# Performance work log

Measured on AMD Instinct MI355X. Metric: run time of the kernel, lower is better.

## Reference

```python
import jax, jax.numpy as jnp
import numpy as np
from jax import lax

B_SZ, SEQ, D_MODEL = 8, 2048, 1024
N_LAYER = 2
D_INNER = 2 * D_MODEL          # expand=2
D_STATE = 16
D_CONV = 4
DT_RANK = D_MODEL // 16        # ceil(1024/16)=64
EPS = 1e-5


def setup_inputs() -> dict:
    key = jax.random.key(0)
    ks = jax.random.split(key, 8)
    f = lambda k, shp, sc: jax.random.normal(k, shp, jnp.float32) * sc
    A_log = jnp.tile(jnp.log(jnp.arange(1, D_STATE + 1, dtype=jnp.float32)),
                     (N_LAYER, D_INNER, 1))  # S4D-real init, [L, d_inner, d_state]
    return {
        "x": f(ks[0], (B_SZ, SEQ, D_MODEL), 1.0),
        "in_proj_w": f(ks[1], (N_LAYER, 2 * D_INNER, D_MODEL), 0.02),
        "conv_w": f(ks[2], (N_LAYER, D_INNER, D_CONV), 0.2),
        "conv_b": jnp.zeros((N_LAYER, D_INNER), jnp.float32),
        "x_proj_w": f(ks[3], (N_LAYER, DT_RANK + 2 * D_STATE, D_INNER), 0.02),
        "dt_proj_w": f(ks[4], (N_LAYER, D_INNER, DT_RANK), 0.1),
        "dt_proj_b": f(ks[5], (N_LAYER, D_INNER), 0.5) - 4.0,  # softplus -> small dt
        "A_log": A_log,
        "D_param": jnp.ones((N_LAYER, D_INNER), jnp.float32),
        "out_proj_w": f(ks[6], (N_LAYER, D_MODEL, D_INNER), 0.02),
        "norm_w": jnp.ones((N_LAYER, D_MODEL), jnp.float32),
        "norm_b": jnp.zeros((N_LAYER, D_MODEL), jnp.float32),
    }


def _layer_norm(x, w, b):
    mu = jnp.mean(x, axis=-1, keepdims=True)
    var = jnp.mean(jnp.square(x - mu), axis=-1, keepdims=True)
    return (x - mu) * lax.rsqrt(var + EPS) * w + b


def _causal_dw_conv(x, w, b):
    # x: [B, Lq, d_inner], w: [d_inner, d_conv] depthwise causal conv
    xp = jnp.pad(x, ((0, 0), (D_CONV - 1, 0), (0, 0)))
    L = x.shape[1]
    y = b
    for k in range(D_CONV):
        y = y + xp[:, k:k + L, :] * w[:, k]
    return y


def _selective_scan(u, dt, Bm, Cm, A, Dp):
    # u, dt: [B, Lq, d_inner]; Bm, Cm: [B, Lq, d_state]; A: [d_inner, d_state]
    def step(h, inp):
        ut, dtt, Bt, Ct = inp                         # [B,di],[B,di],[B,ds],[B,ds]
        dA = jnp.exp(dtt[..., None] * A)              # [B, di, ds]
        h = dA * h + (dtt * ut)[..., None] * Bt[:, None, :]
        y = jnp.einsum('bds,bs->bd', h, Ct)
        return h, y

    h0 = jnp.zeros((u.shape[0], D_INNER, D_STATE), u.dtype)
    xs = (u.transpose(1, 0, 2), dt.transpose(1, 0, 2),
          Bm.transpose(1, 0, 2), Cm.transpose(1, 0, 2))
    _, ys = lax.scan(step, h0, xs)                    # ys: [Lq, B, di]
    return ys.transpose(1, 0, 2) + u * Dp


def _mamba(x, in_w, cw, cb, xpw, dtw, dtb, A_log, Dp, ow):
    xz = jnp.einsum('bld,ed->ble', x, in_w)           # [B, L, 2*d_inner]
    xi, z = jnp.split(xz, 2, axis=-1)
    xc = jax.nn.silu(_causal_dw_conv(xi, cw, cb))     # [B, L, d_inner]
    xdbl = jnp.einsum('bld,ed->ble', xc, xpw)         # [B, L, dt_rank+2*d_state]
    dt_low = xdbl[..., :DT_RANK]
    Bm = xdbl[..., DT_RANK:DT_RANK + D_STATE]
    Cm = xdbl[..., DT_RANK + D_STATE:]
    dt = jax.nn.softplus(jnp.einsum('blr,dr->bld', dt_low, dtw) + dtb)
    A = -jnp.exp(A_log)                               # [d_inner, d_state]
    y = _selective_scan(xc, dt, Bm, Cm, A, Dp)
    y = y * jax.nn.silu(z)
    return jnp.einsum('ble,de->bld', y, ow)           # [B, L, d_model]


def reference(x, in_proj_w, conv_w, conv_b, x_proj_w, dt_proj_w, dt_proj_b,
              A_log, D_param, out_proj_w, norm_w, norm_b):
    residual = None
    for l in range(N_LAYER):
        residual = x if residual is None else x + residual
        h = _layer_norm(residual, norm_w[l], norm_b[l])
        x = _mamba(h, in_proj_w[l], conv_w[l], conv_b[l], x_proj_w[l],
                   dt_proj_w[l], dt_proj_b[l], A_log[l], D_param[l], out_proj_w[l])
    # NOTE: source forward returns x without applying norm_f
    return x
```

## Files before the change

kernel.cpp:

```cpp
#include <hip/hip_runtime.h>
#include <cstddef>
#include <cstdint>

#define SEQB   8
#define SEQL   2048
#define DMODEL 1024
#define DINNER 2048
#define DSTATE 16
#define NC     32
#define TC     64
#define TT     8

typedef __attribute__((ext_vector_type(4))) float f32x4;
typedef __attribute__((ext_vector_type(8))) short bf16x8;
typedef unsigned int u32;
typedef const __attribute__((address_space(1))) u32* gas_ptr;
typedef __attribute__((address_space(3))) u32* las_ptr;

__device__ __forceinline__ void gld16(const void* g, void* l){
  __builtin_amdgcn_global_load_lds((gas_ptr)g, (las_ptr)l, 16, 0, 0);
}

__device__ __forceinline__ float siluf(float x){ return x / (1.f + __expf(-x)); }
__device__ __forceinline__ float softplusf(float x){ return (x > 20.f) ? x : log1pf(__expf(x)); }

__device__ __forceinline__ unsigned short f2bf_rne(float f){
  unsigned int u = __float_as_uint(f);
  u += 0x7FFFu + ((u>>16)&1u);
  return (unsigned short)(u>>16);
}
__device__ __forceinline__ void split_bf(float f, unsigned short& h, unsigned short& l){
  unsigned short hs = f2bf_rne(f);
  float hf = __uint_as_float(((unsigned int)hs)<<16);
  h = hs;
  l = f2bf_rne(f - hf);
}

#define CV8P(PH, PSRC) { \
  const float4* _p4 = (const float4*)(PSRC); \
  float4 _a = _p4[0], _b = _p4[1]; \
  bf16x8 _H, _L; unsigned short _h,_l; \
  split_bf(_a.x,_h,_l); _H[0]=(short)_h; _L[0]=(short)_l; \
  split_bf(_a.y,_h,_l); _H[1]=(short)_h; _L[1]=(short)_l; \
  split_bf(_a.z,_h,_l); _H[2]=(short)_h; _L[2]=(short)_l; \
  split_bf(_a.w,_h,_l); _H[3]=(short)_h; _L[3]=(short)_l; \
  split_bf(_b.x,_h,_l); _H[4]=(short)_h; _L[4]=(short)_l; \
  split_bf(_b.y,_h,_l); _H[5]=(short)_h; _L[5]=(short)_l; \
  split_bf(_b.z,_h,_l); _H[6]=(short)_h; _L[6]=(short)_l; \
  split_bf(_b.w,_h,_l); _H[7]=(short)_h; _L[7]=(short)_l; \
  *(bf16x8*)(PH) = _H; *(bf16x8*)((unsigned short*)(PH) + 64) = _L; }

__global__ __launch_bounds__(256)
void wsplit2(const float* __restrict__ src, unsigned short* __restrict__ dst,
             int K, int k4shift)
{
  int idx = blockIdx.x*256 + threadIdx.x;
  int r  = idx >> k4shift;
  int c4 = idx & ((1<<k4shift)-1);
  float4 v = ((const float4*)src)[idx];
  unsigned short h,l; short4 h4, l4;
  split_bf(v.x,h,l); h4.x=(short)h; l4.x=(short)l;
  split_bf(v.y,h,l); h4.y=(short)h; l4.y=(short)l;
  split_bf(v.z,h,l); h4.z=(short)h; l4.z=(short)l;
  split_bf(v.w,h,l); h4.w=(short)h; l4.w=(short)l;
  size_t ro = (size_t)r*2*K;
  *(short4*)&dst[ro + (c4<<2)]     = h4;
  *(short4*)&dst[ro + K + (c4<<2)] = l4;
}

__global__ __launch_bounds__(256)
void wsplit_og(const float* __restrict__ src, unsigned short* __restrict__ dst)
{
  int idx = blockIdx.x*256 + threadIdx.x;
  int r  = idx >> 9;
  int c4 = idx & 511;
  int layer = r >> 10, rr = r & 1023;
  float4 v = ((const float4*)src)[idx];
  unsigned short h,l; short4 h4, l4;
  split_bf(v.x,h,l); h4.x=(short)h; l4.x=(short)l;
  split_bf(v.y,h,l); h4.y=(short)h; l4.y=(short)l;
  split_bf(v.z,h,l); h4.z=(short)h; l4.z=(short)l;
  split_bf(v.w,h,l); h4.w=(short)h; l4.w=(short)l;
  int col = c4 << 2;
  int g = col >> 8, j = col & 255;
  size_t base = (size_t)layer*1024*4096 + (size_t)rr*4096 + g*512 + j;
  *(short4*)&dst[base]       = h4;
  *(short4*)&dst[base + 256] = l4;
}

__global__ __launch_bounds__(256)
void ln_split2(const float* __restrict__ a, const float* __restrict__ res,
               const float* __restrict__ w, const float* __restrict__ bias,
               unsigned short* __restrict__ Hs)
{
  int row = blockIdx.x;
  size_t off = (size_t)row * DMODEL;
  float4 v = ((const float4*)(a + off))[threadIdx.x];
  if (res){
    float4 u = ((const float4*)(res + off))[threadIdx.x];
    v.x += u.x; v.y += u.y; v.z += u.z; v.w += u.w;
  }
  float s  = v.x + v.y + v.z + v.w;
  float s2 = fmaf(v.x,v.x, fmaf(v.y,v.y, fmaf(v.z,v.z, v.w*v.w)));
  #pragma unroll
  for (int o=32;o>0;o>>=1){ s += __shfl_down(s,o,64); s2 += __shfl_down(s2,o,64); }
  __shared__ float red[8];
  int lane = threadIdx.x & 63, wid = threadIdx.x >> 6;
  if (lane==0){ red[wid]=s; red[4+wid]=s2; }
  __syncthreads();
  s  = red[0]+red[1]+red[2]+red[3];
  s2 = red[4]+red[5]+red[6]+red[7];
  float mu  = s * (1.f/DMODEL);
  float var = s2 * (1.f/DMODEL) - mu*mu;
  float rstd = rsqrtf(var + 1e-5f);
  float4 wv = ((const float4*)w)[threadIdx.x];
  float4 bv = ((const float4*)bias)[threadIdx.x];
  float4 o4;
  o4.x = (v.x-mu)*rstd*wv.x + bv.x;
  o4.y = (v.y-mu)*rstd*wv.y + bv.y;
  o4.z = (v.z-mu)*rstd*wv.z + bv.z;
  o4.w = (v.w-mu)*rstd*wv.w + bv.w;
  unsigned short h,l; short4 h4, l4;
  split_bf(o4.x,h,l); h4.x=(short)h; l4.x=(short)l;
  split_bf(o4.y,h,l); h4.y=(short)h; l4.y=(short)l;
  split_bf(o4.z,h,l); h4.z=(short)h; l4.z=(short)l;
  split_bf(o4.w,h,l); h4.w=(short)h; l4.w=(short)l;
  size_t ro = (size_t)row*2048;
  int c = threadIdx.x<<2;
  *(short4*)&Hs[ro + c]        = h4;
  *(short4*)&Hs[ro + 1024 + c] = l4;
}

__global__ __launch_bounds__(256)
void mgemm_in(const unsigned short* __restrict__ A,
              const unsigned short* __restrict__ B,
              float* __restrict__ XI, float* __restrict__ ZB)
{
  __shared__ __align__(16) unsigned short As[128*64];
  __shared__ __align__(16) unsigned short Bs[128*64];
  const int t = threadIdx.x;
  const int mbase = blockIdx.y << 7, nbase = blockIdx.x << 7;

  const int lane = t & 63, w = t >> 6;
  const int wr = w >> 1, wc = w & 1;
  const int l16 = lane & 15, kq = lane >> 4;

  const int sr8 = lane >> 3, sl8 = lane & 7;
  const unsigned short* pA[4]; const unsigned short* pB[4];
  unsigned short* dA[4]; unsigned short* dB[4];
  #pragma unroll
  for (int c=0;c<4;c++){
    int row = c*32 + w*8 + sr8;
    int ss  = sl8 ^ (row & 7);
    int colb = (ss < 4) ? (ss<<3) : (1024 + ((ss-4)<<3));
    pA[c] = A + (size_t)(mbase+row)*2048 + colb;
    pB[c] = B + (size_t)(nbase+row)*2048 + colb;
    dA[c] = &As[row*64 + sl8*8];
    dB[c] = &Bs[row*64 + sl8*8];
  }

  f32x4 acc[4][4];
  #pragma unroll
  for (int i=0;i<4;i++)
    #pragma unroll
    for (int j=0;j<4;j++) acc[i][j] = (f32x4){0.f,0.f,0.f,0.f};

  for (int k0=0; k0<1024; k0+=32){
    #pragma unroll
    for (int c=0;c<4;c++){
      gld16(pA[c] + k0, dA[c]);
      gld16(pB[c] + k0, dB[c]);
    }
    __syncthreads();
    bf16x8 ah[4], al[4];
    #pragma unroll
    for (int mf=0; mf<4; mf++){
      int ra = wr*64 + mf*16 + l16;
      ah[mf] = *(const bf16x8*)&As[ra*64 + (( kq      ^ (ra&7))<<3)];
      al[mf] = *(const bf16x8*)&As[ra*64 + (((kq+4)   ^ (ra&7))<<3)];
    }
    #pragma unroll
    for (int nf=0; nf<4; nf++){
      int rb = wc*64 + nf*16 + l16;
      bf16x8 bh = *(const bf16x8*)&Bs[rb*64 + (( kq    ^ (rb&7))<<3)];
      bf16x8 bl = *(const bf16x8*)&Bs[rb*64 + (((kq+4) ^ (rb&7))<<3)];
      #pragma unroll
      for (int mf=0; mf<4; mf++){
        acc[mf][nf] = __builtin_amdgcn_mfma_f32_16x16x32_bf16(ah[mf], bh, acc[mf][nf], 0,0,0);
        acc[mf][nf] = __builtin_amdgcn_mfma_f32_16x16x32_bf16(ah[mf], bl, acc[mf][nf], 0,0,0);
        acc[mf][nf] = __builtin_amdgcn_mfma_f32_16x16x32_bf16(al[mf], bh, acc[mf][nf], 0,0,0);
      }
    }
    __syncthreads();
  }

  float* Cd = (nbase < 2048) ? XI : ZB;
  const int cb = (nbase < 2048) ? nbase : (nbase - 2048);
  #pragma unroll
  for (int mf=0; mf<4; mf++){
    int r0 = mbase + wr*64 + mf*16 + kq*4;
    #pragma unroll
    for (int nf=0; nf<4; nf++){
      int c = cb + wc*64 + nf*16 + l16;
      #pragma unroll
      for (int r=0;r<4;r++)
        Cd[(size_t)(r0+r)*2048 + c] = acc[mf][nf][r];
    }
  }
}

__global__ __launch_bounds__(256)
void mgemm_out3(const unsigned short* __restrict__ A,
                const unsigned short* __restrict__ B,
                float* __restrict__ C)
{
  __shared__ __align__(16) unsigned short As[128*64];
  __shared__ __align__(16) unsigned short Bs[128*64];
  const int t = threadIdx.x;
  const int mbase = blockIdx.y << 7, nbase = blockIdx.x << 7;

  const int lane = t & 63, w = t >> 6;
  const int wr = w >> 1, wc = w & 1;
  const int l16 = lane & 15, kq = lane >> 4;

  const int sr8 = lane >> 3, sl8 = lane & 7;
  const unsigned short* pA[4]; const unsigned short* pB[4];
  unsigned short* dA[4]; unsigned short* dB[4];
  #pragma unroll
  for (int c=0;c<4;c++){
    int row = c*32 + w*8 + sr8;
    int ss  = sl8 ^ (row & 7);
    int pofs = (ss < 4) ? (ss<<3) : (256 + ((ss-4)<<3));
    pA[c] = A + (size_t)(mbase+row)*4096 + pofs;
    pB[c] = B + (size_t)(nbase+row)*4096 + pofs;
    dA[c] = &As[row*64 + sl8*8];
    dB[c] = &Bs[row*64 + sl8*8];
  }

  f32x4 acc[4][4];
  #pragma unroll
  for (int i=0;i<4;i++)
    #pragma unroll
    for (int j=0;j<4;j++) acc[i][j] = (f32x4){0.f,0.f,0.f,0.f};

  for (int k0=0; k0<2048; k0+=32){
    const int gso = ((k0>>8)<<9) + (k0 & 255);
    #pragma unroll
    for (int c=0;c<4;c++){
      gld16(pA[c] + gso, dA[c]);
      gld16(pB[c] + gso, dB[c]);
    }
    __syncthreads();
    bf16x8 ah[4], al[4];
    #pragma unroll
    for (int mf=0; mf<4; mf++){
      int ra = wr*64 + mf*16 + l16;
      ah[mf] = *(const bf16x8*)&As[ra*64 + (( kq      ^ (ra&7))<<3)];
      al[mf] = *(const bf16x8*)&As[ra*64 + (((kq+4)   ^ (ra&7))<<3)];
    }
    #pragma unroll
    for (int nf=0; nf<4; nf++){
      int rb = wc*64 + nf*16 + l16;
      bf16x8 bh = *(const bf16x8*)&Bs[rb*64 + (( kq    ^ (rb&7))<<3)];
      bf16x8 bl = *(const bf16x8*)&Bs[rb*64 + (((kq+4) ^ (rb&7))<<3)];
      #pragma unroll
      for (int mf=0; mf<4; mf++){
        acc[mf][nf] = __builtin_amdgcn_mfma_f32_16x16x32_bf16(ah[mf], bh, acc[mf][nf], 0,0,0);
        acc[mf][nf] = __builtin_amdgcn_mfma_f32_16x16x32_bf16(ah[mf], bl, acc[mf][nf], 0,0,0);
        acc[mf][nf] = __builtin_amdgcn_mfma_f32_16x16x32_bf16(al[mf], bh, acc[mf][nf], 0,0,0);
      }
    }
    __syncthreads();
  }

  #pragma unroll
  for (int mf=0; mf<4; mf++){
    int r0 = mbase + wr*64 + mf*16 + kq*4;
    #pragma unroll
    for (int nf=0; nf<4; nf++){
      int c = nbase + wc*64 + nf*16 + l16;
      #pragma unroll
      for (int r=0;r<4;r++)
        C[(size_t)(r0+r)*1024 + c] = acc[mf][nf][r];
    }
  }
}

__global__ __launch_bounds__(256)
void xproj_pair(const unsigned short* __restrict__ A,
                const unsigned short* __restrict__ W2,
                float* __restrict__ XD)
{
  __shared__ __align__(16) unsigned short S[128*64];
  const int t = threadIdx.x;
  const int mbase = blockIdx.x << 5;
  const int lane = t & 63, w = t >> 6;
  const int mf = w & 1, nc0 = (w >> 1) * 48;
  const int l16 = lane & 15, kq = lane >> 4;

  const unsigned short* ps[4]; unsigned short* ds[4];
  #pragma unroll
  for (int c=0;c<4;c++){
    int idx = c*256 + t;
    int row = idx >> 3, sl8 = idx & 7;
    int ss  = sl8 ^ (row & 7);
    int colb = (ss < 4) ? (ss<<3) : (2048 + ((ss-4)<<3));
    ps[c] = (row < 32) ? (A + (size_t)(mbase+row)*4096 + colb)
                       : (W2 + (size_t)(row-32)*4096 + colb);
    ds[c] = &S[row*64 + sl8*8];
  }

  f32x4 acc[3];
  #pragma unroll
  for (int j=0;j<3;j++) acc[j] = (f32x4){0.f,0.f,0.f,0.f};

  for (int k0=0; k0<2048; k0+=32){
    #pragma unroll
    for (int c=0;c<4;c++) gld16(ps[c] + k0, ds[c]);
    __syncthreads();
    int ra = mf*16 + l16;
    bf16x8 ah = *(const bf16x8*)&S[ra*64 + (( kq    ^ (ra&7))<<3)];
    bf16x8 al = *(const bf16x8*)&S[ra*64 + (((kq+4) ^ (ra&7))<<3)];
    #pragma unroll
    for (int nf=0; nf<3; nf++){
      int rb = 32 + nc0 + nf*16 + l16;
      bf16x8 bh = *(const bf16x8*)&S[rb*64 + (( kq    ^ (rb&7))<<3)];
      bf16x8 bl = *(const bf16x8*)&S[rb*64 + (((kq+4) ^ (rb&7))<<3)];
      acc[nf] = __builtin_amdgcn_mfma_f32_16x16x32_bf16(ah, bh, acc[nf], 0,0,0);
      acc[nf] = __builtin_amdgcn_mfma_f32_16x16x32_bf16(ah, bl, acc[nf], 0,0,0);
      acc[nf] = __builtin_amdgcn_mfma_f32_16x16x32_bf16(al, bh, acc[nf], 0,0,0);
    }
    __syncthreads();
  }
  #pragma unroll
  for (int nf=0; nf<3; nf++){
    int c = nc0 + nf*16 + l16;
    int r0s = mbase + mf*16 + kq*4;
    #pragma unroll
    for (int r=0;r<4;r++)
      XD[(size_t)(r0s+r)*96 + c] = acc[nf][r];
  }
}

__global__ __launch_bounds__(256)
void mgemm_dt2(const float* __restrict__ XDf,
               const unsigned short* __restrict__ DTW2,
               float* __restrict__ XI,
               const float* __restrict__ dtb)
{
  __shared__ __align__(16) unsigned short As[128*128];
  __shared__ __align__(16) unsigned short Bs[128*128];
  const int t = threadIdx.x;
  const int mbase = blockIdx.y << 7, nbase = blockIdx.x << 7;
  const int lane = t & 63, w = t >> 6;
  const int wr = w >> 1, wc = w & 1;
  const int l16 = lane & 15, kq = lane >> 4;

  {
    const int row = t >> 1, half = (t & 1) << 5;
    const int r7 = row & 7;
    const float* src = XDf + (size_t)(mbase + row)*96 + half;
    #pragma unroll
    for (int i=0;i<4;i++){
      int g = (half >> 3) + i;
      CV8P(&As[row*128 + ((g ^ r7)<<3)], src + i*8);
    }
  }
  {
    #pragma unroll
    for (int q=0;q<8;q++){
      int idx = q*256 + t;
      int row = idx >> 4, sl = idx & 15;
      int ss  = (sl & 8) | ((sl & 7) ^ (row & 7));
      int col = (ss < 8) ? (ss<<3) : (64 + ((ss-8)<<3));
      gld16(DTW2 + (size_t)(nbase+row)*128 + col, &Bs[row*128 + sl*8]);
    }
  }
  __syncthreads();

  f32x4 acc[4][4];
  #pragma unroll
  for (int i=0;i<4;i++)
    #pragma unroll
    for (int j=0;j<4;j++) acc[i][j] = (f32x4){0.f,0.f,0.f,0.f};

  #pragma unroll
  for (int kb=0; kb<3; kb++){
    const int aoff = (kb==2) ? 8 : 0;
    const int boff = (kb==1) ? 8 : 0;
    #pragma unroll
    for (int kw=0; kw<2; kw++){
      const int sbase = kw*4 + kq;
      bf16x8 af[4];
      #pragma unroll
      for (int mf=0; mf<4; mf++){
        int ra = wr*64 + mf*16 + l16;
        int sA = ((sbase ^ (ra&7)) + aoff);
        af[mf] = *(const bf16x8*)&As[ra*128 + (sA<<3)];
      }
      #pragma unroll
      for (int nf=0; nf<4; nf++){
        int rb = wc*64 + nf*16 + l16;
        int sB = ((sbase ^ (rb&7)) + boff);
        bf16x8 bfr = *(const bf16x8*)&Bs[rb*128 + (sB<<3)];
        #pragma unroll
        for (int mf=0; mf<4; mf++)
          acc[mf][nf] = __builtin_amdgcn_mfma_f32_16x16x32_bf16(af[mf], bfr, acc[mf][nf], 0,0,0);
      }
    }
  }

  #pragma unroll
  for (int mf=0; mf<4; mf++){
    int r0 = mbase + wr*64 + mf*16 + kq*4;
    #pragma unroll
    for (int nf=0; nf<4; nf++){
      int c = nbase + wc*64 + nf*16 + l16;
      float eb = dtb[c];
      #pragma unroll
      for (int r=0;r<4;r++)
        XI[(size_t)(r0+r)*2048 + c] = softplusf(acc[mf][nf][r] + eb);
    }
  }
}

__global__ __launch_bounds__(256)
void conv_silu4(const float* __restrict__ xi, const float* __restrict__ cw,
                const float* __restrict__ cb, unsigned short* __restrict__ u2)
{
  const int r0 = blockIdx.x << 2;
  const int d0 = threadIdx.x << 3;
  const int tt0 = r0 & (SEQL-1);

  float wk[4][8];
  {
    const float4* cw4 = (const float4*)(cw + (size_t)d0*4);
    #pragma unroll
    for (int j=0;j<8;j++){
      float4 wj = cw4[j];
      wk[0][j]=wj.x; wk[1][j]=wj.y; wk[2][j]=wj.z; wk[3][j]=wj.w;
    }
  }
  float bias[8];
  *(float4*)&bias[0] = *(const float4*)(cb + d0);
  *(float4*)&bias[4] = *(const float4*)(cb + d0 + 4);

  float v[7][8];
#define LD8(dst, p) { *(float4*)&dst[0] = ((const float4*)(p))[0]; \
                      *(float4*)&dst[4] = ((const float4*)(p))[1]; }
  #pragma unroll
  for (int k=0;k<7;k++){
    int trel = tt0 - 3 + k;
    if (trel >= 0){
      LD8(v[k], xi + (size_t)(r0 - 3 + k)*DINNER + d0);
    } else {
      #pragma unroll
      for (int j=0;j<8;j++) v[k][j] = 0.f;
    }
  }
#undef LD8

  #pragma unroll
  for (int jrow=0; jrow<4; jrow++){
    unsigned short h8[8], l8[8];
    #pragma unroll
    for (int j=0;j<8;j++){
      float y = fmaf(v[jrow+3][j], wk[3][j], fmaf(v[jrow+2][j], wk[2][j],
                fmaf(v[jrow+1][j], wk[1][j], fmaf(v[jrow][j], wk[0][j], bias[j]))));
      float uv = siluf(y);
      split_bf(uv, h8[j], l8[j]);
    }
    unsigned short* outp = u2 + (size_t)(r0 + jrow)*4096 + d0;
    *(uint4*)outp          = *(const uint4*)h8;
    *(uint4*)(outp + 2048) = *(const uint4*)l8;
  }
}

template<int PASS>
__global__ __launch_bounds__(256)
void scan_chunk(const unsigned short* __restrict__ u2, float* __restrict__ dty,
                const float* __restrict__ xdbl, const float* __restrict__ zb,
                const float* __restrict__ A_log, const float* __restrict__ Dp,
                float* __restrict__ hfin, float* __restrict__ sumdt)
{
  __shared__ __align__(16) float Tdt[2][TT][256];
  __shared__ __align__(16) float Tu [2][TT][256];
  __shared__ __align__(16) float Tz [(PASS==3)?2:1][(PASS==3)?TT:1][(PASS==3)?256:4];
  __shared__ __align__(16) float Tbc[2][TT][32];

  const int tid = threadIdx.x;
  const int idx = blockIdx.x*256 + tid;
  const int d = idx & (DINNER-1);
  const int g = idx >> 11;
  const int cck = g & (NC-1);
  const int bb = g >> 5;
  const int wv = tid >> 6, ln = tid & 63;
  const int dbase = (blockIdx.x << 8) & (DINNER-1);

  float A2[16];
  {
    const float* al = A_log + (size_t)d*DSTATE;
    #pragma unroll
    for (int s=0;s<16;s++) A2[s] = -expf(al[s]) * 1.44269504f;
  }
  float h[16];
  if (PASS == 1){
    #pragma unroll
    for (int s=0;s<16;s++) h[s] = 0.f;
  } else {
    const float* hp = hfin + ((size_t)g*DINNER + d)*16;
    #pragma unroll
    for (int s=0;s<16;s+=4) *(float4*)&h[s] = *(const float4*)(hp + s);
  }
  const float Dv = (PASS==3) ? Dp[d] : 0.f;

  const size_t row0 = (size_t)bb*SEQL + (size_t)cck*TC;

#define STAGE(buf, T0) do { \
    _Pragma("unroll") \
    for (int q=0;q<2;q++){ \
      int r = q*4 + wv; \
      size_t rowi = row0 + (T0) + r; \
      gld16(dty + rowi*2048 + dbase + ln*4, &Tdt[buf][r][0]); \
      const unsigned short* us = u2 + rowi*4096 + \
          ((ln < 32) ? (dbase + ln*8) : (2048 + dbase + (ln-32)*8)); \
      gld16(us, &Tu[buf][r][0]); \
      if (PASS==3) gld16(zb + rowi*2048 + dbase + ln*4, &Tz[buf][r][0]); \
    } \
    if (wv == 3){ \
      gld16(xdbl + (row0 + (T0) + (ln>>3))*96 + 64 + (ln&7)*4, &Tbc[buf][0][0]); \
    } \
  } while(0)

  STAGE(0, 0);
  asm volatile("s_waitcnt vmcnt(0)" ::: "memory");
  __builtin_amdgcn_s_barrier();
  __builtin_amdgcn_sched_barrier(0);

  float sdt = 0.f;

  for (int t0 = 0; t0 < TC; t0 += TT){
    const int cur = (t0 >> 3) & 1, nxt = cur ^ 1;
    const bool hasNext = (t0 + TT < TC);
    if (hasNext) STAGE(nxt, t0 + TT);

    if (hasNext){
      if (PASS==3){
        if (wv==3) asm volatile("s_waitcnt vmcnt(7)" ::: "memory");
        else       asm volatile("s_waitcnt vmcnt(6)" ::: "memory");
      } else {
        if (wv==3) asm volatile("s_waitcnt vmcnt(5)" ::: "memory");
        else       asm volatile("s_waitcnt vmcnt(4)" ::: "memory");
      }
    } else {
      asm volatile("s_waitcnt vmcnt(0)" ::: "memory");
    }
    __builtin_amdgcn_s_barrier();
    __builtin_amdgcn_sched_barrier(0);

    #pragma unroll
    for (int tt=0; tt<TT; tt++){
      float dtc = Tdt[cur][tt][tid];
      const unsigned short* tur = (const unsigned short*)&Tu[cur][tt][0];
      float uc = __uint_as_float((u32)tur[tid] << 16)
               + __uint_as_float((u32)tur[256+tid] << 16);
      float Bv[16], Cv[16];
      #pragma unroll
      for (int q=0;q<4;q++) *(float4*)&Bv[q*4] = *(const float4*)&Tbc[cur][tt][q*4];
      if (PASS==3){
        #pragma unroll
        for (int q=0;q<4;q++) *(float4*)&Cv[q*4] = *(const float4*)&Tbc[cur][tt][16+q*4];
      }
      if (PASS==1) sdt += dtc;
      float du = dtc*uc;
      float y = 0.f;
      #pragma unroll
      for (int s=0;s<16;s++){
        float dA = exp2f(dtc*A2[s]);
        h[s] = fmaf(dA, h[s], du*Bv[s]);
        if (PASS==3) y = fmaf(h[s], Cv[s], y);
      }
      if (PASS==3){
        float zc = Tz[cur][tt][tid];
        y = fmaf(uc, Dv, y);
        float gv = y * siluf(zc);
        unsigned short gh, gl;
        split_bf(gv, gh, gl);
        Tdt[cur][tt][tid] = __uint_as_float((u32)gh | ((u32)gl << 16));
      }
    }

    if (PASS==3) asm volatile("s_waitcnt lgkmcnt(0)" ::: "memory");
    __builtin_amdgcn_s_barrier();
    __builtin_amdgcn_sched_barrier(0);

    if (PASS==3){
      #pragma unroll
      for (int q=0;q<2;q++){
        int r = q*4 + wv;
        size_t rowi = row0 + t0 + r;
        const u32* T = (const u32*)&Tdt[cur][r][0];
        int o0 = ln*4;
        u32 vals[4];
        if (ln < 32){
          #pragma unroll
          for (int k=0;k<4;k++){
            int i2 = (o0+k)*2;
            vals[k] = (T[i2] & 0xFFFFu) | (T[i2+1] << 16);
          }
        } else {
          #pragma unroll
          for (int k=0;k<4;k++){
            int i2 = (o0+k-128)*2;
            vals[k] = (T[i2] >> 16) | (T[i2+1] & 0xFFFF0000u);
          }
        }
        *(float4*)(dty + rowi*2048 + dbase + o0) = *(const float4*)vals;
      }
    }
  }
#undef STAGE

  if (PASS==1){
    float* hp = hfin + ((size_t)g*DINNER + d)*16;
    #pragma unroll
    for (int s=0;s<16;s+=4) *(float4*)(hp + s) = *(const float4*)&h[s];
    sumdt[(size_t)g*DINNER + d] = sdt;
  }
}

__global__ __launch_bounds__(256)
void scan_prop(const float* __restrict__ A_log, float* __restrict__ hfin,
               const float* __restrict__ sumdt)
{
  int idx = blockIdx.x*256 + threadIdx.x;
  int s = idx & 15;
  int d = (idx >> 4) & (DINNER-1);
  int b = idx >> 15;
  float A2 = -expf(A_log[(size_t)d*DSTATE + s]) * 1.44269504f;
  float H = 0.f;
  size_t hbase = ((size_t)b*NC*DINNER + d)*16 + s;
  size_t sbase = (size_t)b*NC*DINNER + d;
  for (int c=0;c<NC;c++){
    float P   = exp2f(A2 * sumdt[sbase + (size_t)c*DINNER]);
    float tmp = hfin[hbase + (size_t)c*DINNER*16];
    hfin[hbase + (size_t)c*DINNER*16] = H;
    H = fmaf(P, H, tmp);
  }
}

extern "C" void kernel_launch(void* const* d_in, const int* in_sizes, int n_in,
                              void* d_out, int out_size, void* d_ws, size_t ws_size,
                              hipStream_t stream)
{
  const float* x    = (const float*)d_in[0];
  const float* in_w = (const float*)d_in[1];
  const float* cw   = (const float*)d_in[2];
  const float* cb   = (const float*)d_in[3];
  const float* xpw  = (const float*)d_in[4];
  const float* dtw  = (const float*)d_in[5];
  const float* dtb  = (const float*)d_in[6];
  const float* A_log= (const float*)d_in[7];
  const float* Dp   = (const float*)d_in[8];
  const float* ow   = (const float*)d_in[9];
  const float* nw   = (const float*)d_in[10];
  const float* nb   = (const float*)d_in[11];
  float* outF = (float*)d_out;

  const size_t fixedB = 33554432ULL + 16777216ULL + 1572864ULL + 1048576ULL;
  const size_t perB   = 58720256ULL;
  int NB = 4;
  while (NB > 1 && fixedB + (size_t)NB*perB > ws_size) NB >>= 1;
  const int Mc = NB * SEQL;
  const int nchunk = SEQB / NB;

  unsigned short* INW2  = (unsigned short*)d_ws;
  unsigned short* OUTWG = INW2 + (size_t)2*4096*2048;
  unsigned short* XPW2  = OUTWG + (size_t)2*1024*4096;
  unsigned short* DTW2  = XPW2 + (size_t)2*96*4096;
  char* dyn = (char*)(DTW2 + (size_t)2*2048*128);

  unsigned short* SH = (unsigned short*)dyn;
  float* XD = (float*)dyn;
  float* HF = (float*)(dyn + (size_t)Mc*384);
  float* SD = (float*)(dyn + (size_t)Mc*2432);
  float* XI = (float*)(dyn + (size_t)Mc*4096);
  float* ZB = XI + (size_t)Mc*2048;
  unsigned short* U2 = (unsigned short*)(ZB + (size_t)Mc*2048);

  wsplit2<<<8192, 256, 0, stream>>>(in_w, INW2, 1024, 8);
  wsplit2<<<384,  256, 0, stream>>>(xpw,  XPW2, 2048, 9);
  wsplit2<<<256,  256, 0, stream>>>(dtw,  DTW2, 64, 4);
  wsplit_og<<<4096, 256, 0, stream>>>(ow, OUTWG);

  for (int c = 0; c < nchunk; ++c){
    const size_t rowoff = (size_t)c * Mc;
    const float* xrows = x + rowoff * DMODEL;
    float* X1 = outF + rowoff * DMODEL;

    for (int l = 0; l < 2; ++l){
      const float* Al = A_log + (size_t)l*DINNER*DSTATE;

      ln_split2<<<Mc, 256, 0, stream>>>(
          (l==0) ? xrows : X1, (l==0) ? nullptr : xrows,
          nw + (size_t)l*DMODEL, nb + (size_t)l*DMODEL, SH);

      mgemm_in<<<dim3(32, Mc/128), 256, 0, stream>>>(
          SH, INW2 + (size_t)l*4096*2048, XI, ZB);

      conv_silu4<<<Mc/4, 256, 0, stream>>>(
          XI, cw + (size_t)l*DINNER*4, cb + (size_t)l*DINNER, U2);

      xproj_pair<<<Mc/32, 256, 0, stream>>>(
          U2, XPW2 + (size_t)l*96*4096, XD);

      mgemm_dt2<<<dim3(16, Mc/128), 256, 0, stream>>>(
          XD, DTW2 + (size_t)l*2048*128, XI, dtb + (size_t)l*DINNER);

      scan_chunk<1><<<NB*NC*8, 256, 0, stream>>>(
          U2, XI, XD, ZB, Al, Dp + (size_t)l*DINNER, HF, SD);
      scan_prop<<<NB*128, 256, 0, stream>>>(Al, HF, SD);
      scan_chunk<3><<<NB*NC*8, 256, 0, stream>>>(
          U2, XI, XD, ZB, Al, Dp + (size_t)l*DINNER, HF, SD);

      mgemm_out3<<<dim3(8, Mc/128), 256, 0, stream>>>(
          (const unsigned short*)XI, OUTWG + (size_t)l*1024*4096, X1);
    }
  }
}
```

Before: 3.159 ms.

## Double-buffer LDS tiles in the in, out and x projection GEMMs

Adds a second LDS buffer to the three bf16-split GEMM kernels so the global-to-LDS load for the next K tile is issued before computing on the current one. Partial vmcnt waits and raw barriers replace __syncthreads. This is meant to hide global load latency behind MFMA work. LDS use per block doubles, which can lower occupancy, and the hand-placed waitcnt and barrier logic risks race conditions if the count assumptions are wrong.

```diff
diff --git a/kernel.cpp b/kernel.cpp
--- a/kernel.cpp
+++ b/kernel.cpp
@@ -136,8 +136,8 @@
               const unsigned short* __restrict__ B,
               float* __restrict__ XI, float* __restrict__ ZB)
 {
-  __shared__ __align__(16) unsigned short As[128*64];
-  __shared__ __align__(16) unsigned short Bs[128*64];
+  __shared__ __align__(16) unsigned short As[2][128*64];
+  __shared__ __align__(16) unsigned short Bs[2][128*64];
   const int t = threadIdx.x;
   const int mbase = blockIdx.y << 7, nbase = blockIdx.x << 7;
 
@@ -147,7 +147,7 @@
 
   const int sr8 = lane >> 3, sl8 = lane & 7;
   const unsigned short* pA[4]; const unsigned short* pB[4];
-  unsigned short* dA[4]; unsigned short* dB[4];
+  int dofs[4];
   #pragma unroll
   for (int c=0;c<4;c++){
     int row = c*32 + w*8 + sr8;
@@ -155,8 +155,7 @@
     int colb = (ss < 4) ? (ss<<3) : (1024 + ((ss-4)<<3));
     pA[c] = A + (size_t)(mbase+row)*2048 + colb;
     pB[c] = B + (size_t)(nbase+row)*2048 + colb;
-    dA[c] = &As[row*64 + sl8*8];
-    dB[c] = &Bs[row*64 + sl8*8];
+    dofs[c] = row*64 + sl8*8;
   }
 
   f32x4 acc[4][4];
@@ -165,25 +164,43 @@
     #pragma unroll
     for (int j=0;j<4;j++) acc[i][j] = (f32x4){0.f,0.f,0.f,0.f};
 
-  for (int k0=0; k0<1024; k0+=32){
-    #pragma unroll
-    for (int c=0;c<4;c++){
-      gld16(pA[c] + k0, dA[c]);
-      gld16(pB[c] + k0, dB[c]);
-    }
-    __syncthreads();
+#define STG(buf, k0) { _Pragma("unroll") \
+    for (int c=0;c<4;c++){ \
+      gld16(pA[c] + (k0), &As[buf][dofs[c]]); \
+      gld16(pB[c] + (k0), &Bs[buf][dofs[c]]); \
+    } }
+
+  STG(0, 0);
+  asm volatile("s_waitcnt vmcnt(0)" ::: "memory");
+  __builtin_amdgcn_s_barrier();
+  __builtin_amdgcn_sched_barrier(0);
+
+  for (int i=0; i<32; i++){
+    const int cur = i & 1, nxt = cur ^ 1;
+    const bool hn = (i+1 < 32);
+    if (hn){
+      STG(nxt, (i+1)*32);
+      asm volatile("s_waitcnt vmcnt(8)" ::: "memory");
+    } else {
+      asm volatile("s_waitcnt vmcnt(0)" ::: "memory");
+    }
+    __builtin_amdgcn_s_barrier();
+    __builtin_amdgcn_sched_barrier(0);
+
+    const unsigned short* Ac = As[cur];
+    const unsigned short* Bc = Bs[cur];
     bf16x8 ah[4], al[4];
     #pragma unroll
     for (int mf=0; mf<4; mf++){
       int ra = wr*64 + mf*16 + l16;
-      ah[mf] = *(const bf16x8*)&As[ra*64 + (( kq      ^ (ra&7))<<3)];
-      al[mf] = *(const bf16x8*)&As[ra*64 + (((kq+4)   ^ (ra&7))<<3)];
+      ah[mf] = *(const bf16x8*)&Ac[ra*64 + (( kq      ^ (ra&7))<<3)];
+      al[mf] = *(const bf16x8*)&Ac[ra*64 + (((kq+4)   ^ (ra&7))<<3)];
     }
     #pragma unroll
     for (int nf=0; nf<4; nf++){
       int rb = wc*64 + nf*16 + l16;
-      bf16x8 bh = *(const bf16x8*)&Bs[rb*64 + (( kq    ^ (rb&7))<<3)];
-      bf16x8 bl = *(const bf16x8*)&Bs[rb*64 + (((kq+4) ^ (rb&7))<<3)];
+      bf16x8 bh = *(const bf16x8*)&Bc[rb*64 + (( kq    ^ (rb&7))<<3)];
+      bf16x8 bl = *(const bf16x8*)&Bc[rb*64 + (((kq+4) ^ (rb&7))<<3)];
       #pragma unroll
       for (int mf=0; mf<4; mf++){
         acc[mf][nf] = __builtin_amdgcn_mfma_f32_16x16x32_bf16(ah[mf], bh, acc[mf][nf], 0,0,0);
@@ -191,8 +208,9 @@
         acc[mf][nf] = __builtin_amdgcn_mfma_f32_16x16x32_bf16(al[mf], bh, acc[mf][nf], 0,0,0);
       }
     }
-    __syncthreads();
-  }
+    __builtin_amdgcn_s_barrier();
+  }
+#undef STG
 
   float* Cd = (nbase < 2048) ? XI : ZB;
   const int cb = (nbase < 2048) ? nbase : (nbase - 2048);
@@ -214,8 +232,8 @@
                 const unsigned short* __restrict__ B,
                 float* __restrict__ C)
 {
-  __shared__ __align__(16) unsigned short As[128*64];
-  __shared__ __align__(16) unsigned short Bs[128*64];
+  __shared__ __align__(16) unsigned short As[2][128*64];
+  __shared__ __align__(16) unsigned short Bs[2][128*64];
   const int t = threadIdx.x;
   const int mbase = blockIdx.y << 7, nbase = blockIdx.x << 7;
 
@@ -225,7 +243,7 @@
 
   const int sr8 = lane >> 3, sl8 = lane & 7;
   const unsigned short* pA[4]; const unsigned short* pB[4];
-  unsigned short* dA[4]; unsigned short* dB[4];
+  int dofs[4];
   #pragma unroll
   for (int c=0;c<4;c++){
     int row = c*32 + w*8 + sr8;
@@ -233,8 +251,7 @@
     int pofs = (ss < 4) ? (ss<<3) : (256 + ((ss-4)<<3));
     pA[c] = A + (size_t)(mbase+row)*4096 + pofs;
     pB[c] = B + (size_t)(nbase+row)*4096 + pofs;
-    dA[c] = &As[row*64 + sl8*8];
-    dB[c] = &Bs[row*64 + sl8*8];
+    dofs[c] = row*64 + sl8*8;
   }
 
   f32x4 acc[4][4];
@@ -243,26 +260,44 @@
     #pragma unroll
     for (int j=0;j<4;j++) acc[i][j] = (f32x4){0.f,0.f,0.f,0.f};
 
-  for (int k0=0; k0<2048; k0+=32){
-    const int gso = ((k0>>8)<<9) + (k0 & 255);
-    #pragma unroll
-    for (int c=0;c<4;c++){
-      gld16(pA[c] + gso, dA[c]);
-      gld16(pB[c] + gso, dB[c]);
-    }
-    __syncthreads();
+#define GSO(i) ((((i)*32)>>8)<<9) + (((i)*32) & 255)
+#define STG(buf, i) { const int gso = GSO(i); _Pragma("unroll") \
+    for (int c=0;c<4;c++){ \
+      gld16(pA[c] + gso, &As[buf][dofs[c]]); \
+      gld16(pB[c] + gso, &Bs[buf][dofs[c]]); \
+    } }
+
+  STG(0, 0);
+  asm volatile("s_waitcnt vmcnt(0)" ::: "memory");
+  __builtin_amdgcn_s_barrier();
+  __builtin_amdgcn_sched_barrier(0);
+
+  for (int i=0; i<64; i++){
+    const int cur = i & 1, nxt = cur ^ 1;
+    const bool hn = (i+1 < 64);
+    if (hn){
+      STG(nxt, i+1);
+      asm volatile("s_waitcnt vmcnt(8)" ::: "memory");
+    } else {
+      asm volatile("s_waitcnt vmcnt(0)" ::: "memory");
+    }
+    __builtin_amdgcn_s_barrier();
+    __builtin_amdgcn_sched_barrier(0);
+
+    const unsigned short* Ac = As[cur];
+    const unsigned short* Bc = Bs[cur];
     bf16x8 ah[4], al[4];
     #pragma unroll
     for (int mf=0; mf<4; mf++){
       int ra = wr*64 + mf*16 + l16;
-      ah[mf] = *(const bf16x8*)&As[ra*64 + (( kq      ^ (ra&7))<<3)];
-      al[mf] = *(const bf16x8*)&As[ra*64 + (((kq+4)   ^ (ra&7))<<3)];
+      ah[mf] = *(const bf16x8*)&Ac[ra*64 + (( kq      ^ (ra&7))<<3)];
+      al[mf] = *(const bf16x8*)&Ac[ra*64 + (((kq+4)   ^ (ra&7))<<3)];
     }
     #pragma unroll
     for (int nf=0; nf<4; nf++){
       int rb = wc*64 + nf*16 + l16;
-      bf16x8 bh = *(const bf16x8*)&Bs[rb*64 + (( kq    ^ (rb&7))<<3)];
-      bf16x8 bl = *(const bf16x8*)&Bs[rb*64 + (((kq+4) ^ (rb&7))<<3)];
+      bf16x8 bh = *(const bf16x8*)&Bc[rb*64 + (( kq    ^ (rb&7))<<3)];
+      bf16x8 bl = *(const bf16x8*)&Bc[rb*64 + (((kq+4) ^ (rb&7))<<3)];
       #pragma unroll
       for (int mf=0; mf<4; mf++){
         acc[mf][nf] = __builtin_amdgcn_mfma_f32_16x16x32_bf16(ah[mf], bh, acc[mf][nf], 0,0,0);
@@ -270,8 +305,10 @@
         acc[mf][nf] = __builtin_amdgcn_mfma_f32_16x16x32_bf16(al[mf], bh, acc[mf][nf], 0,0,0);
       }
     }
-    __syncthreads();
-  }
+    __builtin_amdgcn_s_barrier();
+  }
+#undef STG
+#undef GSO
 
   #pragma unroll
   for (int mf=0; mf<4; mf++){
@@ -291,14 +328,14 @@
                 const unsigned short* __restrict__ W2,
                 float* __restrict__ XD)
 {
-  __shared__ __align__(16) unsigned short S[128*64];
+  __shared__ __align__(16) unsigned short S[2][128*64];
   const int t = threadIdx.x;
   const int mbase = blockIdx.x << 5;
   const int lane = t & 63, w = t >> 6;
   const int mf = w & 1, nc0 = (w >> 1) * 48;
   const int l16 = lane & 15, kq = lane >> 4;
 
-  const unsigned short* ps[4]; unsigned short* ds[4];
+  const unsigned short* ps[4]; int dofs[4];
   #pragma unroll
   for (int c=0;c<4;c++){
     int idx = c*256 + t;
@@ -307,31 +344,50 @@
     int colb = (ss < 4) ? (ss<<3) : (2048 + ((ss-4)<<3));
     ps[c] = (row < 32) ? (A + (size_t)(mbase+row)*4096 + colb)
                        : (W2 + (size_t)(row-32)*4096 + colb);
-    ds[c] = &S[row*64 + sl8*8];
+    dofs[c] = row*64 + sl8*8;
   }
 
   f32x4 acc[3];
   #pragma unroll
   for (int j=0;j<3;j++) acc[j] = (f32x4){0.f,0.f,0.f,0.f};
 
-  for (int k0=0; k0<2048; k0+=32){
-    #pragma unroll
-    for (int c=0;c<4;c++) gld16(ps[c] + k0, ds[c]);
-    __syncthreads();
+#define STG(buf, k0) { _Pragma("unroll") \
+    for (int c=0;c<4;c++) gld16(ps[c] + (k0), &S[buf][dofs[c]]); }
+
+  STG(0, 0);
+  asm volatile("s_waitcnt vmcnt(0)" ::: "memory");
+  __builtin_amdgcn_s_barrier();
+  __builtin_amdgcn_sched_barrier(0);
+
+  for (int i=0; i<64; i++){
+    const int cur = i & 1, nxt = cur ^ 1;
+    const bool hn = (i+1 < 64);
+    if (hn){
+      STG(nxt, (i+1)*32);
+      asm volatile("s_waitcnt vmcnt(4)" ::: "memory");
+    } else {
+      asm volatile("s_waitcnt vmcnt(0)" ::: "memory");
+    }
+    __builtin_amdgcn_s_barrier();
+    __builtin_amdgcn_sched_barrier(0);
+
+    const unsigned short* Sc = S[cur];
     int ra = mf*16 + l16;
-    bf16x8 ah = *(const bf16x8*)&S[ra*64 + (( kq    ^ (ra&7))<<3)];
-    bf16x8 al = *(const bf16x8*)&S[ra*64 + (((kq+4) ^ (ra&7))<<3)];
+    bf16x8 ah = *(const bf16x8*)&Sc[ra*64 + (( kq    ^ (ra&7))<<3)];
+    bf16x8 al = *(const bf16x8*)&Sc[ra*64 + (((kq+4) ^ (ra&7))<<3)];
     #pragma unroll
     for (int nf=0; nf<3; nf++){
       int rb = 32 + nc0 + nf*16 + l16;
-      bf16x8 bh = *(const bf16x8*)&S[rb*64 + (( kq    ^ (rb&7))<<3)];
-      bf16x8 bl = *(const bf16x8*)&S[rb*64 + (((kq+4) ^ (rb&7))<<3)];
+      bf16x8 bh = *(const bf16x8*)&Sc[rb*64 + (( kq    ^ (rb&7))<<3)];
+      bf16x8 bl = *(const bf16x8*)&Sc[rb*64 + (((kq+4) ^ (rb&7))<<3)];
       acc[nf] = __builtin_amdgcn_mfma_f32_16x16x32_bf16(ah, bh, acc[nf], 0,0,0);
       acc[nf] = __builtin_amdgcn_mfma_f32_16x16x32_bf16(ah, bl, acc[nf], 0,0,0);
       acc[nf] = __builtin_amdgcn_mfma_f32_16x16x32_bf16(al, bh, acc[nf], 0,0,0);
     }
-    __syncthreads();
-  }
+    __builtin_amdgcn_s_barrier();
+  }
+#undef STG
+
   #pragma unroll
   for (int nf=0; nf<3; nf++){
     int c = nc0 + nf*16 + l16;
```

New measurement: 3.055 ms. -3.3%, faster.
